# Optimization experiments

Hardware: AMD Instinct MI355X
Metric: run time of the kernel (lower is better)

The kernel has to match this reference:

```python
import jax, jax.numpy as jnp
import numpy as np

B, D, K, N = 32, 512, 64, 1024
EPS = 1e-12  # torch F.normalize eps


def setup_inputs() -> dict:
    key = jax.random.key(0)
    k1, k2, k3 = jax.random.split(key, 3)
    x = jax.random.normal(k1, (B, D, N), dtype=jnp.float32)
    conv_w = jax.random.normal(k2, (K, D), dtype=jnp.float32) * (1.0 / np.sqrt(D))
    centers = jax.random.normal(k3, (D, K), dtype=jnp.float32)
    return {"x": x, "conv_w": conv_w, "centers": centers}


def reference(x, conv_w, centers):
    # scores: 1x1 conv over flattened spatial dim -> [B, K, N]
    scores = jnp.einsum('kd,bdn->bkn', conv_w, x)
    assign = jax.nn.softmax(scores, axis=1)                 # softmax over clusters
    # Algebraic rewrite of sum_n assign[b,k,n] * (x[b,d,n] - centers[d,k]):
    vlad = (jnp.einsum('bdn,bkn->bdk', x, assign)
            - centers[None, :, :] * assign.sum(axis=-1)[:, None, :])  # [B, D, K]
    # intra-normalization over descriptor dim D (F.normalize with eps clamp)
    vlad = vlad / jnp.maximum(jnp.linalg.norm(vlad, axis=1, keepdims=True), EPS)
    desc = vlad.reshape(vlad.shape[0], -1)                  # [B, D*K]
    desc = desc / jnp.maximum(jnp.linalg.norm(desc, axis=1, keepdims=True), EPS)
    return desc
```

## Files before the change

### kernel.cpp

```cpp
#include <hip/hip_runtime.h>
#include <hip/hip_bf16.h>

#define Bv 32
#define Dv 512
#define Kv 64
#define Nv 1024
#define EPSv 1e-12f

typedef __attribute__((ext_vector_type(8))) short bf16x8;
typedef __attribute__((ext_vector_type(4))) float f32x4;

__device__ __forceinline__ unsigned short f2b(float f) {
  union { float f; unsigned u; } v; v.f = f;
  unsigned r = v.u + 0x7fffu + ((v.u >> 16) & 1u);
  return (unsigned short)(r >> 16);
}
__device__ __forceinline__ unsigned pack2(float a, float b) {
  return (unsigned)f2b(a) | ((unsigned)f2b(b) << 16);
}

__global__ __launch_bounds__(256) void wconv(const float* __restrict__ w,
                                             unsigned short* __restrict__ wbf,
                                             float* __restrict__ zbuf) {
  int id = blockIdx.x * 256 + threadIdx.x;
  int i = id * 4;
  float4 v = *(const float4*)&w[i];
  uint2 o = make_uint2(pack2(v.x, v.y), pack2(v.z, v.w));
  *(uint2*)&wbf[i] = o;
  if (id < 2 * Bv * Kv) zbuf[id] = 0.f;
}

__global__ __launch_bounds__(512) void fused_scores(
    const float* __restrict__ x, const unsigned short* __restrict__ wbf,
    unsigned short* __restrict__ xbf, unsigned short* __restrict__ assign,
    float* __restrict__ asum) {
  __shared__ unsigned short xT[64 * 520];
  __shared__ float redmax[4][64];
  __shared__ float redsum[4][64];

  const int t = threadIdx.x;
  const int b = blockIdx.y;
  const int nt = blockIdx.x;
  const int n0 = nt * 64;

  {
    const int lo = t & 15;
    const int hi = t >> 4;
    const int s = (lo >> 1) & 3;
    const float* xb = x + (size_t)b * Dv * Nv + n0;
    unsigned short* xt = xbf + ((size_t)b * 16 + nt) * (Dv * 64);
#pragma unroll
    for (int r = 0; r < 8; r++) {
      int d = (hi + 32 * r) * 2;
      int n4 = lo * 4;
      float4 v0 = *(const float4*)&xb[(size_t)d * Nv + n4];
      float4 v1 = *(const float4*)&xb[(size_t)(d + 1) * Nv + n4];
      *(uint2*)&xt[(size_t)d * 64 + n4] =
          make_uint2(pack2(v0.x, v0.y), pack2(v0.z, v0.w));
      *(uint2*)&xt[(size_t)(d + 1) * 64 + n4] =
          make_uint2(pack2(v1.x, v1.y), pack2(v1.z, v1.w));
      unsigned w0 = pack2(v0.x, v1.x);
      unsigned w1 = pack2(v0.y, v1.y);
      unsigned w2 = pack2(v0.z, v1.z);
      unsigned w3 = pack2(v0.w, v1.w);
      unsigned a0 = (s & 1) ? w1 : w0, a1 = (s & 1) ? w2 : w1,
               a2 = (s & 1) ? w3 : w2, a3 = (s & 1) ? w0 : w3;
      unsigned b0 = (s & 2) ? a2 : a0, b1 = (s & 2) ? a3 : a1,
               b2 = (s & 2) ? a0 : a2, b3 = (s & 2) ? a1 : a3;
      *(unsigned*)&xT[(n4 + ((0 + s) & 3)) * 520 + d] = b0;
      *(unsigned*)&xT[(n4 + ((1 + s) & 3)) * 520 + d] = b1;
      *(unsigned*)&xT[(n4 + ((2 + s) & 3)) * 520 + d] = b2;
      *(unsigned*)&xT[(n4 + ((3 + s) & 3)) * 520 + d] = b3;
    }
  }
  __syncthreads();

  const int wv = t >> 6;
  const int lane = t & 63;
  const int q = lane >> 4;
  const int m = lane & 15;
  const int k16 = wv & 3;
  const int nsub = wv >> 2;

  f32x4 acc0 = {0.f, 0.f, 0.f, 0.f};
  f32x4 acc1 = {0.f, 0.f, 0.f, 0.f};

  const unsigned short* wp = wbf + (size_t)(k16 * 16 + m) * Dv + q * 8;
  const unsigned short* l0 = &xT[(nsub * 32 + m) * 520 + q * 8];
  const unsigned short* l1 = l0 + 16 * 520;

#pragma unroll
  for (int d0 = 0; d0 < Dv; d0 += 32) {
    bf16x8 af = *(const bf16x8*)(wp + d0);
    bf16x8 bf0 = *(const bf16x8*)(l0 + d0);
    bf16x8 bf1 = *(const bf16x8*)(l1 + d0);
    acc0 = __builtin_amdgcn_mfma_f32_16x16x32_bf16(af, bf0, acc0, 0, 0, 0);
    acc1 = __builtin_amdgcn_mfma_f32_16x16x32_bf16(af, bf1, acc1, 0, 0, 0);
  }

  float m0 = fmaxf(fmaxf(acc0[0], acc0[1]), fmaxf(acc0[2], acc0[3]));
  float m1 = fmaxf(fmaxf(acc1[0], acc1[1]), fmaxf(acc1[2], acc1[3]));
  m0 = fmaxf(m0, __shfl_xor(m0, 16)); m0 = fmaxf(m0, __shfl_xor(m0, 32));
  m1 = fmaxf(m1, __shfl_xor(m1, 16)); m1 = fmaxf(m1, __shfl_xor(m1, 32));
  if (q == 0) {
    redmax[k16][nsub * 32 + m] = m0;
    redmax[k16][nsub * 32 + 16 + m] = m1;
  }
  __syncthreads();
  const int c0 = nsub * 32 + m, c1 = c0 + 16;
  float mc0 = fmaxf(fmaxf(redmax[0][c0], redmax[1][c0]), fmaxf(redmax[2][c0], redmax[3][c0]));
  float mc1 = fmaxf(fmaxf(redmax[0][c1], redmax[1][c1]), fmaxf(redmax[2][c1], redmax[3][c1]));

  float e0[4], e1[4];
  float s0 = 0.f, s1 = 0.f;
#pragma unroll
  for (int r = 0; r < 4; r++) {
    e0[r] = __expf(acc0[r] - mc0); s0 += e0[r];
    e1[r] = __expf(acc1[r] - mc1); s1 += e1[r];
  }
  s0 += __shfl_xor(s0, 16); s0 += __shfl_xor(s0, 32);
  s1 += __shfl_xor(s1, 16); s1 += __shfl_xor(s1, 32);
  if (q == 0) {
    redsum[k16][c0] = s0;
    redsum[k16][c1] = s1;
  }
  __syncthreads();
  float sc0 = 1.0f / (redsum[0][c0] + redsum[1][c0] + redsum[2][c0] + redsum[3][c0]);
  float sc1 = 1.0f / (redsum[0][c1] + redsum[1][c1] + redsum[2][c1] + redsum[3][c1]);

  unsigned short* at_ = assign + ((size_t)b * 16 + nt) * (Kv * 64)
                        + (size_t)(k16 * 16 + q * 4) * 64 + nsub * 32;
#pragma unroll
  for (int r = 0; r < 4; r++) {
    float v0 = e0[r] * sc0;
    float v1 = e1[r] * sc1;
    at_[r * 64 + m] = f2b(v0);
    at_[r * 64 + 16 + m] = f2b(v1);
    float p = v0 + v1;
    p += __shfl_xor(p, 1); p += __shfl_xor(p, 2);
    p += __shfl_xor(p, 4); p += __shfl_xor(p, 8);
    if (m == 0) atomicAdd(&asum[b * Kv + k16 * 16 + q * 4 + r], p);
  }
}

__global__ __launch_bounds__(512, 2) void vlad_mfma(
    const unsigned short* __restrict__ xbf, const unsigned short* __restrict__ assign,
    const float* __restrict__ centers, const float* __restrict__ asum,
    float* __restrict__ vlad, float* __restrict__ colsq) {
  __shared__ float sred[4][64][4];

  const int t = threadIdx.x;
  const int flat = blockIdx.x;
  const int loc = flat >> 3;
  const int b = ((loc >> 5) << 3) + (flat & 7);
  const int d0 = (loc & 31) * 16;
  const int wv = t >> 6;
  const int ksub = wv & 3;
  const int nh = wv >> 2;
  const int lane = t & 63;
  const int q = lane >> 4;
  const int m = lane & 15;
  const int k16 = ksub * 16;

  const unsigned short* xp = xbf + ((size_t)b * 16 + nh * 8) * (Dv * 64)
                             + (size_t)(d0 + m) * 64 + q * 8;
  const unsigned short* ap = assign + ((size_t)b * 16 + nh * 8) * (Kv * 64)
                             + (size_t)(k16 + m) * 64 + q * 8;

  f32x4 acc = {0.f, 0.f, 0.f, 0.f};
  bf16x8 xv[8], av[8];

#pragma unroll
  for (int i = 0; i < 8; i++) {
    xv[i] = *(const bf16x8*)(xp + (i >> 1) * (Dv * 64) + (i & 1) * 32);
    av[i] = *(const bf16x8*)(ap + (i >> 1) * (Kv * 64) + (i & 1) * 32);
  }
  __builtin_amdgcn_sched_barrier(0);

#pragma unroll
  for (int i = 0; i < 8; i++) {
    acc = __builtin_amdgcn_mfma_f32_16x16x32_bf16(xv[i], av[i], acc, 0, 0, 0);
    xv[i] = *(const bf16x8*)(xp + ((i + 8) >> 1) * (Dv * 64) + (i & 1) * 32);
    av[i] = *(const bf16x8*)(ap + ((i + 8) >> 1) * (Kv * 64) + (i & 1) * 32);
    __builtin_amdgcn_sched_barrier(0);
  }

#pragma unroll
  for (int i = 0; i < 8; i++)
    acc = __builtin_amdgcn_mfma_f32_16x16x32_bf16(xv[i], av[i], acc, 0, 0, 0);

  if (nh == 1) {
#pragma unroll
    for (int r = 0; r < 4; r++) sred[ksub][lane][r] = acc[r];
  }
  __syncthreads();
  if (nh == 0) {
    const int k = k16 + m;
    const float as = asum[b * Kv + k];
    float ss = 0.f;
#pragma unroll
    for (int r = 0; r < 4; r++) {
      float v = acc[r] + sred[ksub][lane][r];
      int d = d0 + q * 4 + r;
      float val = v - centers[d * Kv + k] * as;
      vlad[((size_t)b * Dv + d) * Kv + k] = val;
      ss = fmaf(val, val, ss);
    }
    ss += __shfl_xor(ss, 16);
    ss += __shfl_xor(ss, 32);
    if (q == 0) atomicAdd(&colsq[b * Kv + k], ss);
  }
}

__global__ __launch_bounds__(256) void scale_kernel(
    const float* __restrict__ vlad, const float* __restrict__ colsq,
    float* __restrict__ out) {
  const int t = threadIdx.x;
  const size_t i = ((size_t)blockIdx.x * 256 + t) * 4;
  const int b = (int)(i >> 15);
  __shared__ float scs[64];
  __shared__ float bsh;
  if (t < 64) {
    float tot = colsq[b * Kv + t];
    float sc = 1.0f / fmaxf(sqrtf(tot), EPSv);
    scs[t] = sc;
    float contrib = tot * sc * sc;
#pragma unroll
    for (int off = 32; off > 0; off >>= 1) contrib += __shfl_down(contrib, off);
    if (t == 0) bsh = 1.0f / fmaxf(sqrtf(contrib), EPSv);
  }
  __syncthreads();
  float4 v = *(const float4*)&vlad[i];
  const int k = (int)(i & 63);
  float4 o;
  o.x = v.x * scs[k + 0] * bsh;
  o.y = v.y * scs[k + 1] * bsh;
  o.z = v.z * scs[k + 2] * bsh;
  o.w = v.w * scs[k + 3] * bsh;
  *(float4*)&out[i] = o;
}

extern "C" void kernel_launch(void* const* d_in, const int* in_sizes, int n_in,
                              void* d_out, int out_size, void* d_ws, size_t ws_size,
                              hipStream_t stream) {
  const float* x = (const float*)d_in[0];
  const float* w = (const float*)d_in[1];
  const float* centers = (const float*)d_in[2];
  float* out = (float*)d_out;

  char* ws = (char*)d_ws;
  unsigned short* assign = (unsigned short*)ws;
  float* vlad = (float*)(ws + 4194304);
  unsigned short* xbf = (unsigned short*)(ws + 8388608);
  unsigned short* wbf = (unsigned short*)(ws + 41943040);
  float* asum = (float*)(ws + 42008576);
  float* colsq = asum + Bv * Kv;

  wconv<<<32, 256, 0, stream>>>(w, wbf, asum);
  fused_scores<<<dim3(Nv / 64, Bv), 512, 0, stream>>>(x, wbf, xbf, assign, asum);
  vlad_mfma<<<1024, 512, 0, stream>>>(xbf, assign, centers, asum, vlad, colsq);
  scale_kernel<<<1024, 256, 0, stream>>>(vlad, colsq, out);
}
```

Baseline: 143.5 us.

## Stage VLAD GEMM tiles through LDS with async global-to-LDS loads, split combine

Replaces the register-direct VLAD MFMA kernel with a double-buffered kernel. It streams 64x64 bf16 tiles of x and assign into LDS via global_load_lds, so each wave reuses the assign tile across four K-subtiles. The N dimension is split in two halves written to a partial buffer, and a new combine kernel sums them, subtracts centers*asum and accumulates column norms. The fused_scores grid is also remapped to a flat index that spreads batches across blocks. This adds a kernel launch and an extra round trip of fp32 partials through memory in exchange for fewer redundant global reads of assign.

```diff
diff --git a/kernel.cpp b/kernel.cpp
--- a/kernel.cpp
+++ b/kernel.cpp
@@ -18,6 +18,11 @@
 __device__ __forceinline__ unsigned pack2(float a, float b) {
   return (unsigned)f2b(a) | ((unsigned)f2b(b) << 16);
 }
+
+#define GLOAD_LDS16(gsrc, ldst)                                             \
+  __builtin_amdgcn_global_load_lds(                                         \
+      (const __attribute__((address_space(1))) void*)(gsrc),                \
+      (__attribute__((address_space(3))) void*)(ldst), 16, 0, 0)
 
 __global__ __launch_bounds__(256) void wconv(const float* __restrict__ w,
                                              unsigned short* __restrict__ wbf,
@@ -39,8 +44,10 @@
   __shared__ float redsum[4][64];
 
   const int t = threadIdx.x;
-  const int b = blockIdx.y;
-  const int nt = blockIdx.x;
+  const int flat = blockIdx.x;
+  const int i0 = flat >> 3;
+  const int b = (flat & 7) + 8 * (i0 & 3);
+  const int nt = i0 >> 2;
   const int n0 = nt * 64;
 
   {
@@ -143,73 +150,113 @@
   }
 }
 
-__global__ __launch_bounds__(512, 2) void vlad_mfma(
+__global__ __launch_bounds__(256) void vlad_stage(
     const unsigned short* __restrict__ xbf, const unsigned short* __restrict__ assign,
-    const float* __restrict__ centers, const float* __restrict__ asum,
-    float* __restrict__ vlad, float* __restrict__ colsq) {
-  __shared__ float sred[4][64][4];
+    float* __restrict__ vpart) {
+  __shared__ unsigned short xs[2][64 * 64];
+  __shared__ unsigned short as_[2][64 * 64];
 
   const int t = threadIdx.x;
   const int flat = blockIdx.x;
-  const int loc = flat >> 3;
-  const int b = ((loc >> 5) << 3) + (flat & 7);
-  const int d0 = (loc & 31) * 16;
-  const int wv = t >> 6;
-  const int ksub = wv & 3;
-  const int nh = wv >> 2;
+  const int i0 = flat >> 3;
+  const int b = (flat & 7) + 8 * (i0 & 3);
+  const int j = i0 >> 2;
+  const int dg = j & 7;
+  const int nh = j >> 3;
+
+  const int w = t >> 6;
   const int lane = t & 63;
   const int q = lane >> 4;
   const int m = lane & 15;
-  const int k16 = ksub * 16;
-
-  const unsigned short* xp = xbf + ((size_t)b * 16 + nh * 8) * (Dv * 64)
-                             + (size_t)(d0 + m) * 64 + q * 8;
-  const unsigned short* ap = assign + ((size_t)b * 16 + nh * 8) * (Kv * 64)
-                             + (size_t)(k16 + m) * 64 + q * 8;
-
-  f32x4 acc = {0.f, 0.f, 0.f, 0.f};
-  bf16x8 xv[8], av[8];
-
-#pragma unroll
-  for (int i = 0; i < 8; i++) {
-    xv[i] = *(const bf16x8*)(xp + (i >> 1) * (Dv * 64) + (i & 1) * 32);
-    av[i] = *(const bf16x8*)(ap + (i >> 1) * (Kv * 64) + (i & 1) * 32);
-  }
-  __builtin_amdgcn_sched_barrier(0);
-
-#pragma unroll
-  for (int i = 0; i < 8; i++) {
-    acc = __builtin_amdgcn_mfma_f32_16x16x32_bf16(xv[i], av[i], acc, 0, 0, 0);
-    xv[i] = *(const bf16x8*)(xp + ((i + 8) >> 1) * (Dv * 64) + (i & 1) * 32);
-    av[i] = *(const bf16x8*)(ap + ((i + 8) >> 1) * (Kv * 64) + (i & 1) * 32);
-    __builtin_amdgcn_sched_barrier(0);
-  }
-
-#pragma unroll
-  for (int i = 0; i < 8; i++)
-    acc = __builtin_amdgcn_mfma_f32_16x16x32_bf16(xv[i], av[i], acc, 0, 0, 0);
-
-  if (nh == 1) {
-#pragma unroll
-    for (int r = 0; r < 4; r++) sred[ksub][lane][r] = acc[r];
-  }
-  __syncthreads();
-  if (nh == 0) {
-    const int k = k16 + m;
-    const float as = asum[b * Kv + k];
-    float ss = 0.f;
-#pragma unroll
-    for (int r = 0; r < 4; r++) {
-      float v = acc[r] + sred[ksub][lane][r];
-      int d = d0 + q * 4 + r;
-      float val = v - centers[d * Kv + k] * as;
-      vlad[((size_t)b * Dv + d) * Kv + k] = val;
-      ss = fmaf(val, val, ss);
+
+  const unsigned short* xsrc = xbf + ((size_t)b * 16 + nh * 8) * (Dv * 64)
+                               + (size_t)dg * 64 * 64;
+  const unsigned short* asrc = assign + ((size_t)b * 16 + nh * 8) * (Kv * 64);
+
+#define STAGE(buf, tt)                                                        \
+  {                                                                           \
+    const unsigned short* _xs = xsrc + (size_t)(tt) * (Dv * 64) + w * 1024;   \
+    const unsigned short* _as = asrc + (size_t)(tt) * (Kv * 64) + w * 1024;   \
+    unsigned short* _lx = &xs[buf][w * 1024];                                 \
+    unsigned short* _la = &as_[buf][w * 1024];                                \
+    GLOAD_LDS16(_xs + lane * 8, _lx);                                         \
+    GLOAD_LDS16(_xs + 512 + lane * 8, _lx + 512);                             \
+    GLOAD_LDS16(_as + lane * 8, _la);                                         \
+    GLOAD_LDS16(_as + 512 + lane * 8, _la + 512);                             \
+  }
+
+  f32x4 acc0 = {0.f,0.f,0.f,0.f}, acc1 = {0.f,0.f,0.f,0.f};
+  f32x4 acc2 = {0.f,0.f,0.f,0.f}, acc3 = {0.f,0.f,0.f,0.f};
+
+  STAGE(0, 0)
+  asm volatile("s_waitcnt vmcnt(0)");
+  __syncthreads();
+
+  int buf = 0;
+#pragma unroll
+  for (int tt = 0; tt < 8; tt++) {
+    if (tt < 7) STAGE(buf ^ 1, tt + 1)
+#pragma unroll
+    for (int nc = 0; nc < 2; nc++) {
+      bf16x8 xv = *(const bf16x8*)&xs[buf][(w * 16 + m) * 64 + nc * 32 + q * 8];
+      bf16x8 a0 = *(const bf16x8*)&as_[buf][(0 * 16 + m) * 64 + nc * 32 + q * 8];
+      bf16x8 a1 = *(const bf16x8*)&as_[buf][(1 * 16 + m) * 64 + nc * 32 + q * 8];
+      bf16x8 a2 = *(const bf16x8*)&as_[buf][(2 * 16 + m) * 64 + nc * 32 + q * 8];
+      bf16x8 a3 = *(const bf16x8*)&as_[buf][(3 * 16 + m) * 64 + nc * 32 + q * 8];
+      acc0 = __builtin_amdgcn_mfma_f32_16x16x32_bf16(xv, a0, acc0, 0, 0, 0);
+      acc1 = __builtin_amdgcn_mfma_f32_16x16x32_bf16(xv, a1, acc1, 0, 0, 0);
+      acc2 = __builtin_amdgcn_mfma_f32_16x16x32_bf16(xv, a2, acc2, 0, 0, 0);
+      acc3 = __builtin_amdgcn_mfma_f32_16x16x32_bf16(xv, a3, acc3, 0, 0, 0);
     }
-    ss += __shfl_xor(ss, 16);
-    ss += __shfl_xor(ss, 32);
-    if (q == 0) atomicAdd(&colsq[b * Kv + k], ss);
-  }
+    asm volatile("s_waitcnt vmcnt(0)");
+    __syncthreads();
+    buf ^= 1;
+  }
+#undef STAGE
+
+  float* vp = vpart + (((size_t)nh * Bv + b) * Dv + dg * 64 + w * 16) * Kv;
+  f32x4 accs[4] = {acc0, acc1, acc2, acc3};
+#pragma unroll
+  for (int ks = 0; ks < 4; ks++)
+#pragma unroll
+    for (int r = 0; r < 4; r++)
+      vp[(size_t)(q * 4 + r) * Kv + ks * 16 + m] = accs[ks][r];
+}
+
+__global__ __launch_bounds__(256) void combine(
+    const float* __restrict__ vpart, const float* __restrict__ centers,
+    const float* __restrict__ asum, float* __restrict__ vlad,
+    float* __restrict__ colsq) {
+  __shared__ float cacc[64];
+  const int t = threadIdx.x;
+  const int flat = blockIdx.x;
+  const int i0 = flat >> 3;
+  const int b = (flat & 7) + 8 * (i0 & 3);
+  const int dblk = i0 >> 2;
+  if (t < 64) cacc[t] = 0.f;
+  __syncthreads();
+
+  const size_t eb = ((size_t)b * Dv + dblk * 16) * Kv;
+  const size_t i = eb + t * 4;
+  const int d = (int)((i >> 6) & 511);
+  const int k0 = (int)(i & 63);
+
+  float4 h0 = *(const float4*)&vpart[i];
+  float4 h1 = *(const float4*)&vpart[(size_t)Bv * Dv * Kv + i];
+  float4 c = *(const float4*)&centers[d * Kv + k0];
+  float4 av = *(const float4*)&asum[b * Kv + k0];
+  float4 o;
+  o.x = h0.x + h1.x - c.x * av.x;
+  o.y = h0.y + h1.y - c.y * av.y;
+  o.z = h0.z + h1.z - c.z * av.z;
+  o.w = h0.w + h1.w - c.w * av.w;
+  *(float4*)&vlad[i] = o;
+  atomicAdd(&cacc[k0 + 0], o.x * o.x);
+  atomicAdd(&cacc[k0 + 1], o.y * o.y);
+  atomicAdd(&cacc[k0 + 2], o.z * o.z);
+  atomicAdd(&cacc[k0 + 3], o.w * o.w);
+  __syncthreads();
+  if (t < 64) atomicAdd(&colsq[b * Kv + t], cacc[t]);
 }
 
 __global__ __launch_bounds__(256) void scale_kernel(
@@ -255,9 +302,11 @@
   unsigned short* wbf = (unsigned short*)(ws + 41943040);
   float* asum = (float*)(ws + 42008576);
   float* colsq = asum + Bv * Kv;
+  float* vpart = (float*)(ws + 42025088);
 
   wconv<<<32, 256, 0, stream>>>(w, wbf, asum);
-  fused_scores<<<dim3(Nv / 64, Bv), 512, 0, stream>>>(x, wbf, xbf, assign, asum);
-  vlad_mfma<<<1024, 512, 0, stream>>>(xbf, assign, centers, asum, vlad, colsq);
+  fused_scores<<<512, 512, 0, stream>>>(x, wbf, xbf, assign, asum);
+  vlad_stage<<<512, 256, 0, stream>>>(xbf, assign, vpart);
+  combine<<<1024, 256, 0, stream>>>(vpart, centers, asum, vlad, colsq);
   scale_kernel<<<1024, 256, 0, stream>>>(vlad, colsq, out);
 }
```

After: 131.6 us. 1.09x faster.

## Stage vlad GEMM tiles through LDS with async global-to-LDS double buffering

Applied to the files above, without the earlier changes.

Replaces the register-direct vlad_mfma kernel with a 256-thread kernel that double-buffers xbf and assign tiles into LDS using global_load_lds, with an XOR swizzle against bank conflicts. Each block now covers 32 d by 64 k over all N, so each wave reuses one x fragment for two MFMAs and the cross-wave reduction through shared memory goes away. Both kernels also get a flattened grid that interleaves batches, intended to improve cache locality. The cost is fewer blocks (512 instead of 1024), a block-wide barrier every stage, and a full vmcnt drain before each barrier.

```diff
diff --git a/kernel.cpp b/kernel.cpp
--- a/kernel.cpp
+++ b/kernel.cpp
@@ -18,6 +18,11 @@
 __device__ __forceinline__ unsigned pack2(float a, float b) {
   return (unsigned)f2b(a) | ((unsigned)f2b(b) << 16);
 }
+
+#define GLOAD_LDS16(gsrc, ldst)                                             \
+  __builtin_amdgcn_global_load_lds(                                         \
+      (const __attribute__((address_space(1))) void*)(gsrc),                \
+      (__attribute__((address_space(3))) void*)(ldst), 16, 0, 0)
 
 __global__ __launch_bounds__(256) void wconv(const float* __restrict__ w,
                                              unsigned short* __restrict__ wbf,
@@ -39,8 +44,10 @@
   __shared__ float redsum[4][64];
 
   const int t = threadIdx.x;
-  const int b = blockIdx.y;
-  const int nt = blockIdx.x;
+  const int flat = blockIdx.x;
+  const int i0 = flat >> 3;
+  const int b = (flat & 7) + 8 * (i0 & 3);
+  const int nt = i0 >> 2;
   const int n0 = nt * 64;
 
   {
@@ -143,72 +150,95 @@
   }
 }
 
-__global__ __launch_bounds__(512, 2) void vlad_mfma(
+__global__ __launch_bounds__(256) void vlad_stage(
     const unsigned short* __restrict__ xbf, const unsigned short* __restrict__ assign,
     const float* __restrict__ centers, const float* __restrict__ asum,
     float* __restrict__ vlad, float* __restrict__ colsq) {
-  __shared__ float sred[4][64][4];
+  __shared__ unsigned short xs[2][2 * 2048];
+  __shared__ unsigned short as_[2][2 * 4096];
 
   const int t = threadIdx.x;
   const int flat = blockIdx.x;
-  const int loc = flat >> 3;
-  const int b = ((loc >> 5) << 3) + (flat & 7);
-  const int d0 = (loc & 31) * 16;
-  const int wv = t >> 6;
-  const int ksub = wv & 3;
-  const int nh = wv >> 2;
+  const int i0 = flat >> 3;
+  const int b = (flat & 7) + 8 * (i0 & 3);
+  const int dg = i0 >> 2;
+
+  const int w = t >> 6;
+  const int dh = w & 1;
+  const int kh = w >> 1;
   const int lane = t & 63;
   const int q = lane >> 4;
   const int m = lane & 15;
-  const int k16 = ksub * 16;
-
-  const unsigned short* xp = xbf + ((size_t)b * 16 + nh * 8) * (Dv * 64)
-                             + (size_t)(d0 + m) * 64 + q * 8;
-  const unsigned short* ap = assign + ((size_t)b * 16 + nh * 8) * (Kv * 64)
-                             + (size_t)(k16 + m) * 64 + q * 8;
-
-  f32x4 acc = {0.f, 0.f, 0.f, 0.f};
-  bf16x8 xv[8], av[8];
-
-#pragma unroll
-  for (int i = 0; i < 8; i++) {
-    xv[i] = *(const bf16x8*)(xp + (i >> 1) * (Dv * 64) + (i & 1) * 32);
-    av[i] = *(const bf16x8*)(ap + (i >> 1) * (Kv * 64) + (i & 1) * 32);
-  }
-  __builtin_amdgcn_sched_barrier(0);
-
-#pragma unroll
-  for (int i = 0; i < 8; i++) {
-    acc = __builtin_amdgcn_mfma_f32_16x16x32_bf16(xv[i], av[i], acc, 0, 0, 0);
-    xv[i] = *(const bf16x8*)(xp + ((i + 8) >> 1) * (Dv * 64) + (i & 1) * 32);
-    av[i] = *(const bf16x8*)(ap + ((i + 8) >> 1) * (Kv * 64) + (i & 1) * 32);
-    __builtin_amdgcn_sched_barrier(0);
-  }
-
-#pragma unroll
-  for (int i = 0; i < 8; i++)
-    acc = __builtin_amdgcn_mfma_f32_16x16x32_bf16(xv[i], av[i], acc, 0, 0, 0);
-
-  if (nh == 1) {
-#pragma unroll
-    for (int r = 0; r < 4; r++) sred[ksub][lane][r] = acc[r];
-  }
-  __syncthreads();
-  if (nh == 0) {
-    const int k = k16 + m;
-    const float as = asum[b * Kv + k];
-    float ss = 0.f;
-#pragma unroll
-    for (int r = 0; r < 4; r++) {
-      float v = acc[r] + sred[ksub][lane][r];
-      int d = d0 + q * 4 + r;
-      float val = v - centers[d * Kv + k] * as;
-      vlad[((size_t)b * Dv + d) * Kv + k] = val;
-      ss = fmaf(val, val, ss);
+
+  const int rs = lane >> 3;
+  const int csw = (lane & 7) ^ (rs & 7);
+
+  const unsigned short* xbase = xbf + (size_t)b * 16 * (Dv * 64) + dg * 2048;
+  const unsigned short* abase = assign + (size_t)b * 16 * (Kv * 64);
+
+#define STAGE(buf, rr)                                                        \
+  {                                                                           \
+    _Pragma("unroll")                                                         \
+    for (int s = 0; s < 2; s++) {                                             \
+      int tile = (rr) * 2 + s;                                                \
+      const unsigned short* _xs = xbase + (size_t)tile * (Dv * 64)            \
+                                  + (w * 8 + rs) * 64 + csw * 8;              \
+      const unsigned short* _a1 = abase + (size_t)tile * (Kv * 64)            \
+                                  + (w * 16 + rs) * 64 + csw * 8;             \
+      GLOAD_LDS16(_xs, &xs[buf][s * 2048 + w * 512]);                         \
+      GLOAD_LDS16(_a1, &as_[buf][s * 4096 + w * 1024]);                       \
+      GLOAD_LDS16(_a1 + 512, &as_[buf][s * 4096 + w * 1024 + 512]);           \
+    }                                                                         \
+  }
+
+  f32x4 acc0 = {0.f,0.f,0.f,0.f}, acc1 = {0.f,0.f,0.f,0.f};
+
+  STAGE(0, 0)
+  asm volatile("s_waitcnt vmcnt(0)");
+  __syncthreads();
+
+  int buf = 0;
+#pragma unroll
+  for (int rr = 0; rr < 8; rr++) {
+    if (rr < 7) STAGE(buf ^ 1, rr + 1)
+#pragma unroll
+    for (int s = 0; s < 2; s++) {
+#pragma unroll
+      for (int nc = 0; nc < 2; nc++) {
+        const int cidx = (((nc * 4 + q) ^ (m & 7))) * 8;
+        bf16x8 xv = *(const bf16x8*)&xs[buf][s * 2048 + (dh * 16 + m) * 64 + cidx];
+        bf16x8 a0 = *(const bf16x8*)&as_[buf][s * 4096 + (kh * 32 + m) * 64 + cidx];
+        bf16x8 a1 = *(const bf16x8*)&as_[buf][s * 4096 + (kh * 32 + 16 + m) * 64 + cidx];
+        acc0 = __builtin_amdgcn_mfma_f32_16x16x32_bf16(xv, a0, acc0, 0, 0, 0);
+        acc1 = __builtin_amdgcn_mfma_f32_16x16x32_bf16(xv, a1, acc1, 0, 0, 0);
+      }
     }
-    ss += __shfl_xor(ss, 16);
-    ss += __shfl_xor(ss, 32);
-    if (q == 0) atomicAdd(&colsq[b * Kv + k], ss);
+    asm volatile("s_waitcnt vmcnt(0)");
+    __syncthreads();
+    buf ^= 1;
+  }
+#undef STAGE
+
+  const int k0 = kh * 32 + m;
+  const int k1 = k0 + 16;
+  const float as0 = asum[b * Kv + k0];
+  const float as1 = asum[b * Kv + k1];
+  float ss0 = 0.f, ss1 = 0.f;
+#pragma unroll
+  for (int r = 0; r < 4; r++) {
+    int d = dg * 32 + dh * 16 + q * 4 + r;
+    float v0 = acc0[r] - centers[d * Kv + k0] * as0;
+    float v1 = acc1[r] - centers[d * Kv + k1] * as1;
+    vlad[((size_t)b * Dv + d) * Kv + k0] = v0;
+    vlad[((size_t)b * Dv + d) * Kv + k1] = v1;
+    ss0 = fmaf(v0, v0, ss0);
+    ss1 = fmaf(v1, v1, ss1);
+  }
+  ss0 += __shfl_xor(ss0, 16); ss0 += __shfl_xor(ss0, 32);
+  ss1 += __shfl_xor(ss1, 16); ss1 += __shfl_xor(ss1, 32);
+  if (q == 0) {
+    atomicAdd(&colsq[b * Kv + k0], ss0);
+    atomicAdd(&colsq[b * Kv + k1], ss1);
   }
 }
 
@@ -257,7 +287,7 @@
   float* colsq = asum + Bv * Kv;
 
   wconv<<<32, 256, 0, stream>>>(w, wbf, asum);
-  fused_scores<<<dim3(Nv / 64, Bv), 512, 0, stream>>>(x, wbf, xbf, assign, asum);
-  vlad_mfma<<<1024, 512, 0, stream>>>(xbf, assign, centers, asum, vlad, colsq);
+  fused_scores<<<512, 512, 0, stream>>>(x, wbf, xbf, assign, asum);
+  vlad_stage<<<512, 256, 0, stream>>>(xbf, assign, centers, asum, vlad, colsq);
   scale_kernel<<<1024, 256, 0, stream>>>(vlad, colsq, out);
 }
```

Result: faster. 124.6 us (-13.2%).
